# Kernel tuning notes

Hardware: AMD Instinct MI355X
Metric: run time of the kernel (lower is better)

## Reference

```python
import jax, jax.numpy as jnp
import numpy as np

B, D, K = 256, 1024, 128  # batch, num variables (leaves), units per node


def setup_inputs() -> dict:
    key = jax.random.key(0)
    k1, k2, k3, k4 = jax.random.split(key, 4)
    x = jax.random.normal(k1, (B, D), dtype=jnp.float32)
    mu = jax.random.normal(k2, (D, K), dtype=jnp.float32)
    log_sigma = 0.1 * jax.random.normal(k3, (D, K), dtype=jnp.float32)
    # log-weight logits for all 512+256+...+1 = 1023 inner sum nodes, concatenated
    weights = jax.random.normal(k4, (D - 1, K, K), dtype=jnp.float32)
    return {"x": x, "mu": mu, "log_sigma": log_sigma, "weights": weights}


def _log_matmul(y, logw):
    # y: [B, d, K] log-values; logw: [d, K, K] normalized log-weights (<= 0)
    # out[b,d,i] = logsumexp_j( logw[d,i,j] + y[b,d,j] ), computed without
    # materializing a [B,d,K,K] tensor: shift-by-max + linear-space matmul.
    m = jnp.max(y, axis=-1, keepdims=True)                  # [B, d, 1]
    e = jnp.exp(y - m)                                      # [B, d, K]
    s = jnp.einsum("bdj,dij->bdi", e, jnp.exp(logw))        # [B, d, K]
    return m + jnp.log(s)


def reference(x, mu, log_sigma, weights):
    # --- input (leaf) layer: per-variable Gaussian log-densities, [B, D, K] ---
    half_log_2pi = 0.5 * jnp.log(jnp.asarray(2.0 * np.pi, dtype=x.dtype))
    z = (x[:, :, None] - mu) * jnp.exp(-log_sigma)
    y = -0.5 * z * z - log_sigma - half_log_2pi             # [B, D, K]

    # --- topological sweep over the binary-tree DAG: product then sum layers ---
    off = 0
    d = y.shape[1]
    while d > 1:
        d //= 2
        # product nodes: sum log-probs of adjacent children -> [B, d, K]
        y = y[:, 0::2, :] + y[:, 1::2, :]
        # sum nodes: normalized log-space mixture over K child units
        logw = jax.nn.log_softmax(weights[off:off + d], axis=-1)  # [d, K, K]
        y = _log_matmul(y, logw)
        off += d
    return y[:, 0, :]  # root outputs, [B, K]
```

## Files before the change

kernel.cpp:

```cpp
#include <hip/hip_runtime.h>
#include <math.h>


#define DD 1024
#define KK 128
#define NT 256
#define HALF_LOG_2PI 0.9189385332046727f

typedef __attribute__((ext_vector_type(8))) short bf16x8;
typedef __attribute__((ext_vector_type(4))) float f32x4;

__device__ __forceinline__ unsigned short bf16_rn(float f) {
    unsigned u = __builtin_bit_cast(unsigned, f);
    u += 0x7fffu + ((u >> 16) & 1u);
    return (unsigned short)(u >> 16);
}
__device__ __forceinline__ float bf16f(unsigned short h) {
    unsigned u = ((unsigned)h) << 16;
    return __builtin_bit_cast(float, u);
}

template <int BT, bool LEAF>
__global__ __launch_bounds__(NT, 1) void spn_level(
    const float* __restrict__ x, const float* __restrict__ mu,
    const float* __restrict__ ls, const float* __restrict__ yprev,
    const float* __restrict__ weights, float* __restrict__ yout,
    int d, int woff)
{
    constexpr int JPT = NT / BT;
    constexpr int JW  = KK / JPT;

    extern __shared__ char smem[];
    unsigned short* Whi = (unsigned short*)smem;
    unsigned short* Wlo = Whi + 128 * 128;
    unsigned short* Ehi = Wlo + 128 * 128;
    unsigned short* Elo = Ehi + BT * 128;
    float* logrs = (float*)(Elo + BT * 128);
    float* mrow  = logrs + 128;
    float* redW  = mrow + BT;
    float* redE  = redW + NT;
    float* musig = redE + NT;

    const int n     = blockIdx.x;
    const int btile = blockIdx.y;
    const int t     = threadIdx.x;

    if (LEAF) {
        const int c = t >> 7, j = t & 127;
        const float lsv = ls[(size_t)(2 * n + c) * KK + j];
        musig[c * 128 + j]       = __expf(-lsv);
        musig[256 + c * 128 + j] = -lsv - HALF_LOG_2PI;
        musig[512 + c * 128 + j] = mu[(size_t)(2 * n + c) * KK + j];
    }
    {
        const int i = t >> 1;
        const int h = t & 1;
        const float* wg = weights + (((size_t)(woff + n)) << 14) + (i << 7) + (h << 6);
        const int sw = (i & 7) << 3;
        unsigned short* wh = Whi + i * 128;
        unsigned short* wl = Wlo + i * 128;
        float ps = 0.f;
        #pragma unroll
        for (int c = 0; c < 8; ++c) {
            float4 v0 = *(const float4*)(wg + 8 * c);
            float4 v1 = *(const float4*)(wg + 8 * c + 4);
            float e[8] = {__expf(v0.x), __expf(v0.y), __expf(v0.z), __expf(v0.w),
                          __expf(v1.x), __expf(v1.y), __expf(v1.z), __expf(v1.w)};
            bf16x8 hv, lv;
            #pragma unroll
            for (int q = 0; q < 8; ++q) {
                ps += e[q];
                const unsigned short hb = bf16_rn(e[q]);
                hv[q] = (short)hb;
                lv[q] = (short)bf16_rn(e[q] - bf16f(hb));
            }
            const int j0 = (h << 6) + 8 * c;
            *(bf16x8*)&wh[j0 ^ sw] = hv;
            *(bf16x8*)&wl[j0 ^ sw] = lv;
        }
        redW[t] = ps;
    }
    __syncthreads();

    if (t < 128) logrs[t] = __logf(redW[2 * t] + redW[2 * t + 1]);

    const int bl = t & (BT - 1);
    const int jh = t / BT;
    const int b  = btile * BT + bl;
    float p[JW];
    float lmax = -3.0e38f;
    if (LEAF) {
        const float xa = x[(size_t)b * DD + 2 * n];
        const float xb = x[(size_t)b * DD + 2 * n + 1];
        const float* isga = musig;        const float* isgb = musig + 128;
        const float* cta  = musig + 256;  const float* ctb  = musig + 384;
        const float* mva  = musig + 512;  const float* mvb  = musig + 640;
        #pragma unroll
        for (int c = 0; c < JW / 4; ++c) {
            const int j = jh * JW + 4 * c;
            const float4 ia = *(const float4*)(isga + j);
            const float4 ib = *(const float4*)(isgb + j);
            const float4 ca = *(const float4*)(cta + j);
            const float4 cb = *(const float4*)(ctb + j);
            const float4 ma = *(const float4*)(mva + j);
            const float4 mb = *(const float4*)(mvb + j);
            float za, zb, v;
            za = (xa - ma.x) * ia.x; zb = (xb - mb.x) * ib.x;
            v = fmaf(-0.5f * za, za, ca.x) + fmaf(-0.5f * zb, zb, cb.x);
            p[4 * c + 0] = v; lmax = fmaxf(lmax, v);
            za = (xa - ma.y) * ia.y; zb = (xb - mb.y) * ib.y;
            v = fmaf(-0.5f * za, za, ca.y) + fmaf(-0.5f * zb, zb, cb.y);
            p[4 * c + 1] = v; lmax = fmaxf(lmax, v);
            za = (xa - ma.z) * ia.z; zb = (xb - mb.z) * ib.z;
            v = fmaf(-0.5f * za, za, ca.z) + fmaf(-0.5f * zb, zb, cb.z);
            p[4 * c + 2] = v; lmax = fmaxf(lmax, v);
            za = (xa - ma.w) * ia.w; zb = (xb - mb.w) * ib.w;
            v = fmaf(-0.5f * za, za, ca.w) + fmaf(-0.5f * zb, zb, cb.w);
            p[4 * c + 3] = v; lmax = fmaxf(lmax, v);
        }
    } else {
        const float* ra = yprev + ((size_t)b * (2 * d) + 2 * n) * KK + jh * JW;
        const float* rb = ra + KK;
        #pragma unroll
        for (int c = 0; c < JW / 4; ++c) {
            const float4 a4 = *(const float4*)(ra + 4 * c);
            const float4 b4 = *(const float4*)(rb + 4 * c);
            const float p0 = a4.x + b4.x, p1 = a4.y + b4.y;
            const float p2 = a4.z + b4.z, p3 = a4.w + b4.w;
            p[4 * c + 0] = p0; p[4 * c + 1] = p1;
            p[4 * c + 2] = p2; p[4 * c + 3] = p3;
            lmax = fmaxf(lmax, fmaxf(fmaxf(p0, p1), fmaxf(p2, p3)));
        }
    }
    redE[t] = lmax;
    __syncthreads();

    if (t < BT) {
        float m = redE[t];
        #pragma unroll
        for (int q = 1; q < JPT; ++q) m = fmaxf(m, redE[t + BT * q]);
        mrow[t] = m;
    }
    float mx = redE[bl];
    #pragma unroll
    for (int q = 1; q < JPT; ++q) mx = fmaxf(mx, redE[bl + BT * q]);
    {
        const int sw = (bl & 7) << 3;
        unsigned short* eh = Ehi + bl * 128;
        unsigned short* el = Elo + bl * 128;
        #pragma unroll
        for (int c = 0; c < JW / 8; ++c) {
            bf16x8 hv, lv;
            #pragma unroll
            for (int q = 0; q < 8; ++q) {
                const float ev = __expf(p[8 * c + q] - mx);
                const unsigned short hb = bf16_rn(ev);
                hv[q] = (short)hb;
                lv[q] = (short)bf16_rn(ev - bf16f(hb));
            }
            const int j0 = jh * JW + 8 * c;
            *(bf16x8*)&eh[j0 ^ sw] = hv;
            *(bf16x8*)&el[j0 ^ sw] = lv;
        }
    }
    __syncthreads();

    const int w  = t >> 6;
    const int ln = t & 63;
    const int lr = ln & 15;
    const int lk = ln >> 4;
    constexpr int NWB = (BT == 128) ? 4 : 1;
    const int bt0 = (BT == 128) ? ((w >> 1) * 4) : (w & 1);
    const int it0 = (BT == 128) ? ((w & 1) * 4) : ((w >> 1) * 4);

    f32x4 acc[NWB][4];
    #pragma unroll
    for (int bi = 0; bi < NWB; ++bi)
        #pragma unroll
        for (int ci = 0; ci < 4; ++ci) acc[bi][ci] = (f32x4){0.f, 0.f, 0.f, 0.f};

    const int kb = lk * 8;
    #pragma unroll
    for (int ks = 0; ks < 4; ++ks) {
        const int jo = ks * 32 + kb;
        bf16x8 ah[NWB], al[NWB];
        #pragma unroll
        for (int bi = 0; bi < NWB; ++bi) {
            const int r = (bt0 + bi) * 16 + lr;
            const int idx = r * 128 + (jo ^ ((r & 7) << 3));
            ah[bi] = *(bf16x8*)&Ehi[idx];
            al[bi] = *(bf16x8*)&Elo[idx];
        }
        #pragma unroll
        for (int ci = 0; ci < 4; ++ci) {
            const int r = (it0 + ci) * 16 + lr;
            const int idx = r * 128 + (jo ^ ((r & 7) << 3));
            const bf16x8 bh = *(bf16x8*)&Whi[idx];
            const bf16x8 blo = *(bf16x8*)&Wlo[idx];
            #pragma unroll
            for (int bi = 0; bi < NWB; ++bi) {
                acc[bi][ci] = __builtin_amdgcn_mfma_f32_16x16x32_bf16(ah[bi], bh,  acc[bi][ci], 0, 0, 0);
                acc[bi][ci] = __builtin_amdgcn_mfma_f32_16x16x32_bf16(ah[bi], blo, acc[bi][ci], 0, 0, 0);
                acc[bi][ci] = __builtin_amdgcn_mfma_f32_16x16x32_bf16(al[bi], bh,  acc[bi][ci], 0, 0, 0);
            }
        }
    }

    #pragma unroll
    for (int bi = 0; bi < NWB; ++bi) {
        const int brl = (bt0 + bi) * 16 + lk * 4;
        #pragma unroll
        for (int ci = 0; ci < 4; ++ci) {
            const int ic = (it0 + ci) * 16 + lr;
            const float lrs = logrs[ic];
            const f32x4 a = acc[bi][ci];
            #pragma unroll
            for (int r = 0; r < 4; ++r) {
                const float m = mrow[brl + r];
                const size_t off = ((size_t)(btile * BT + brl + r) * d + n) * KK + ic;
                yout[off] = m + __logf(a[r]) - lrs;
            }
        }
    }
}

extern "C" void kernel_launch(void* const* d_in, const int* in_sizes, int n_in,
                              void* d_out, int out_size, void* d_ws, size_t ws_size,
                              hipStream_t stream) {
    const float* x  = (const float*)d_in[0];
    const float* mu = (const float*)d_in[1];
    const float* ls = (const float*)d_in[2];
    const float* w  = (const float*)d_in[3];
    float* out  = (float*)d_out;
    float* buf0 = (float*)d_ws;
    float* buf1 = buf0 + (size_t)256 * 512 * KK;

    const int sh128 = 65536 + 128 * 512 + 512 + 512 + 1024 + 1024 + 3072;
    const int sh32  = 65536 +  32 * 512 + 512 + 128 + 1024 + 1024 + 3072;

    (void)hipFuncSetAttribute((const void*)spn_level<128, true>,
                              hipFuncAttributeMaxDynamicSharedMemorySize, sh128);
    (void)hipFuncSetAttribute((const void*)spn_level<128, false>,
                              hipFuncAttributeMaxDynamicSharedMemorySize, sh128);
    (void)hipFuncSetAttribute((const void*)spn_level<32, false>,
                              hipFuncAttributeMaxDynamicSharedMemorySize, sh32);

    spn_level<128, true><<<dim3(512, 2), dim3(NT), sh128, stream>>>(
        x, mu, ls, nullptr, w, buf0, 512, 0);

    const float* src = buf0;
    float* other = buf1;
    int woff = 512;
    for (int d = 256; d >= 1; d >>= 1) {
        float* o = (d == 1) ? out : other;
        if (d >= 64) {
            spn_level<128, false><<<dim3(d, 2), dim3(NT), sh128, stream>>>(
                nullptr, nullptr, nullptr, src, w, o, d, woff);
        } else {
            spn_level<32, false><<<dim3(d, 8), dim3(NT), sh32, stream>>>(
                nullptr, nullptr, nullptr, src, w, o, d, woff);
        }
        woff += d;
        other = (float*)src;
        src = o;
    }
}
```

Measured before the change: 268.4 us.

## Precompute split-bf16 weights in a pre-pass and double threads per block

Adds a w_pre kernel that exponentiates all sum-node weights once, splits them into hi/lo bf16 planes in the swizzled layout, and stores per-row log-sums to workspace. The level kernels then copy these planes straight into LDS with global_load_lds instead of doing exp and conversion per block, which removes repeated transcendental work when several batch tiles share a node. Block size goes from 256 to 512 threads with launch bounds allowing 2 blocks per CU, and the MFMA work per wave is cut to match. The cost is an extra kernel launch and extra workspace traffic for the bf16 planes; the fused path remains as a fallback when the workspace is too small.

```diff
diff --git a/kernel.cpp b/kernel.cpp
--- a/kernel.cpp
+++ b/kernel.cpp
@@ -4,7 +4,7 @@
 
 #define DD 1024
 #define KK 128
-#define NT 256
+#define NT 512
 #define HALF_LOG_2PI 0.9189385332046727f
 
 typedef __attribute__((ext_vector_type(8))) short bf16x8;
@@ -19,12 +19,54 @@
     unsigned u = ((unsigned)h) << 16;
     return __builtin_bit_cast(float, u);
 }
-
-template <int BT, bool LEAF>
-__global__ __launch_bounds__(NT, 1) void spn_level(
+__device__ __forceinline__ void gload_lds16(const void* g, void* l) {
+    __builtin_amdgcn_global_load_lds(
+        (const __attribute__((address_space(1))) unsigned int*)g,
+        (__attribute__((address_space(3))) unsigned int*)l, 16, 0, 0);
+}
+
+__global__ __launch_bounds__(256, 4) void w_pre(
+    const float* __restrict__ weights, unsigned short* __restrict__ wpl,
+    float* __restrict__ lrs)
+{
+    __shared__ float red[256];
+    const int node = blockIdx.x;
+    const int t = threadIdx.x;
+    const int i = t >> 1, h = t & 1;
+    const float* wg = weights + ((size_t)node << 14) + (i << 7) + (h << 6);
+    unsigned short* wh = wpl + ((size_t)node << 15) + i * 128;
+    unsigned short* wl = wh + 16384;
+    const int sw = (i & 7) << 3;
+    float ps = 0.f;
+    #pragma unroll
+    for (int c = 0; c < 8; ++c) {
+        float4 v0 = *(const float4*)(wg + 8 * c);
+        float4 v1 = *(const float4*)(wg + 8 * c + 4);
+        float e[8] = {__expf(v0.x), __expf(v0.y), __expf(v0.z), __expf(v0.w),
+                      __expf(v1.x), __expf(v1.y), __expf(v1.z), __expf(v1.w)};
+        bf16x8 hv, lv;
+        #pragma unroll
+        for (int q = 0; q < 8; ++q) {
+            ps += e[q];
+            const unsigned short hb = bf16_rn(e[q]);
+            hv[q] = (short)hb;
+            lv[q] = (short)bf16_rn(e[q] - bf16f(hb));
+        }
+        const int j0 = (h << 6) + 8 * c;
+        *(bf16x8*)&wh[j0 ^ sw] = hv;
+        *(bf16x8*)&wl[j0 ^ sw] = lv;
+    }
+    red[t] = ps;
+    __syncthreads();
+    if (t < 128) lrs[(size_t)node * 128 + t] = __logf(red[2 * t] + red[2 * t + 1]);
+}
+
+template <int BT, bool LEAF, bool PRE>
+__global__ __launch_bounds__(NT, 2) void spn_level(
     const float* __restrict__ x, const float* __restrict__ mu,
     const float* __restrict__ ls, const float* __restrict__ yprev,
-    const float* __restrict__ weights, float* __restrict__ yout,
+    const float* __restrict__ weights, const unsigned short* __restrict__ wpl,
+    const float* __restrict__ lrsg, float* __restrict__ yout,
     int d, int woff)
 {
     constexpr int JPT = NT / BT;
@@ -32,36 +74,37 @@
 
     extern __shared__ char smem[];
     unsigned short* Whi = (unsigned short*)smem;
-    unsigned short* Wlo = Whi + 128 * 128;
-    unsigned short* Ehi = Wlo + 128 * 128;
+    unsigned short* Wlo = Whi + 16384;
+    unsigned short* Ehi = Wlo + 16384;
     unsigned short* Elo = Ehi + BT * 128;
     float* logrs = (float*)(Elo + BT * 128);
     float* mrow  = logrs + 128;
-    float* redW  = mrow + BT;
-    float* redE  = redW + NT;
-    float* musig = redE + NT;
+    float* redE  = mrow + BT;
+    float* redW  = redE + NT;
+    float* musig = redW + NT;
 
     const int n     = blockIdx.x;
     const int btile = blockIdx.y;
     const int t     = threadIdx.x;
-
-    if (LEAF) {
-        const int c = t >> 7, j = t & 127;
-        const float lsv = ls[(size_t)(2 * n + c) * KK + j];
-        musig[c * 128 + j]       = __expf(-lsv);
-        musig[256 + c * 128 + j] = -lsv - HALF_LOG_2PI;
-        musig[512 + c * 128 + j] = mu[(size_t)(2 * n + c) * KK + j];
-    }
-    {
-        const int i = t >> 1;
-        const int h = t & 1;
-        const float* wg = weights + (((size_t)(woff + n)) << 14) + (i << 7) + (h << 6);
-        const int sw = (i & 7) << 3;
+    const int node  = woff + n;
+
+    if (PRE) {
+        const int wv = t >> 6, ln = t & 63;
+        const char* gsrc = (const char*)(wpl + ((size_t)node << 15)) + wv * 8192 + (size_t)ln * 16;
+        char* ldst = (char*)Whi + wv * 8192;
+        #pragma unroll
+        for (int q = 0; q < 8; ++q)
+            gload_lds16(gsrc + q * 1024, ldst + q * 1024);
+        if (t < 128) logrs[t] = lrsg[(size_t)node * 128 + t];
+    } else {
+        const int i = t >> 2, h = t & 3;
+        const float* wg = weights + ((size_t)node << 14) + (i << 7) + (h << 5);
         unsigned short* wh = Whi + i * 128;
         unsigned short* wl = Wlo + i * 128;
+        const int sw = (i & 7) << 3;
         float ps = 0.f;
         #pragma unroll
-        for (int c = 0; c < 8; ++c) {
+        for (int c = 0; c < 4; ++c) {
             float4 v0 = *(const float4*)(wg + 8 * c);
             float4 v1 = *(const float4*)(wg + 8 * c + 4);
             float e[8] = {__expf(v0.x), __expf(v0.y), __expf(v0.z), __expf(v0.w),
@@ -74,15 +117,23 @@
                 hv[q] = (short)hb;
                 lv[q] = (short)bf16_rn(e[q] - bf16f(hb));
             }
-            const int j0 = (h << 6) + 8 * c;
+            const int j0 = (h << 5) + 8 * c;
             *(bf16x8*)&wh[j0 ^ sw] = hv;
             *(bf16x8*)&wl[j0 ^ sw] = lv;
         }
         redW[t] = ps;
     }
+    if (LEAF && t < 256) {
+        const int c = t >> 7, j = t & 127;
+        const float lsv = ls[(size_t)(2 * n + c) * KK + j];
+        musig[c * 128 + j]       = __expf(-lsv);
+        musig[256 + c * 128 + j] = -lsv - HALF_LOG_2PI;
+        musig[512 + c * 128 + j] = mu[(size_t)(2 * n + c) * KK + j];
+    }
     __syncthreads();
 
-    if (t < 128) logrs[t] = __logf(redW[2 * t] + redW[2 * t + 1]);
+    if (!PRE && t < 128)
+        logrs[t] = __logf(redW[4 * t] + redW[4 * t + 1] + redW[4 * t + 2] + redW[4 * t + 3]);
 
     const int bl = t & (BT - 1);
     const int jh = t / BT;
@@ -165,19 +216,22 @@
     }
     __syncthreads();
 
-    const int w  = t >> 6;
+    const int wv = t >> 6;
     const int ln = t & 63;
     const int lr = ln & 15;
     const int lk = ln >> 4;
-    constexpr int NWB = (BT == 128) ? 4 : 1;
-    const int bt0 = (BT == 128) ? ((w >> 1) * 4) : (w & 1);
-    const int it0 = (BT == 128) ? ((w & 1) * 4) : ((w >> 1) * 4);
-
-    f32x4 acc[NWB][4];
+    constexpr int NWB = (BT == 128) ? 2 : 1;
+    constexpr int NCI = (BT == 128) ? 4 : 2;
+    const int wr = (BT == 128) ? (wv >> 1) : (wv & 1);
+    const int wc = (BT == 128) ? (wv & 1) : (wv >> 1);
+    const int bt0 = wr * NWB;
+    const int it0 = wc * NCI;
+
+    f32x4 acc[NWB][NCI];
     #pragma unroll
     for (int bi = 0; bi < NWB; ++bi)
         #pragma unroll
-        for (int ci = 0; ci < 4; ++ci) acc[bi][ci] = (f32x4){0.f, 0.f, 0.f, 0.f};
+        for (int ci = 0; ci < NCI; ++ci) acc[bi][ci] = (f32x4){0.f, 0.f, 0.f, 0.f};
 
     const int kb = lk * 8;
     #pragma unroll
@@ -192,10 +246,10 @@
             al[bi] = *(bf16x8*)&Elo[idx];
         }
         #pragma unroll
-        for (int ci = 0; ci < 4; ++ci) {
+        for (int ci = 0; ci < NCI; ++ci) {
             const int r = (it0 + ci) * 16 + lr;
             const int idx = r * 128 + (jo ^ ((r & 7) << 3));
-            const bf16x8 bh = *(bf16x8*)&Whi[idx];
+            const bf16x8 bh  = *(bf16x8*)&Whi[idx];
             const bf16x8 blo = *(bf16x8*)&Wlo[idx];
             #pragma unroll
             for (int bi = 0; bi < NWB; ++bi) {
@@ -210,15 +264,15 @@
     for (int bi = 0; bi < NWB; ++bi) {
         const int brl = (bt0 + bi) * 16 + lk * 4;
         #pragma unroll
-        for (int ci = 0; ci < 4; ++ci) {
+        for (int ci = 0; ci < NCI; ++ci) {
             const int ic = (it0 + ci) * 16 + lr;
-            const float lrs = logrs[ic];
+            const float lrsv = logrs[ic];
             const f32x4 a = acc[bi][ci];
             #pragma unroll
             for (int r = 0; r < 4; ++r) {
                 const float m = mrow[brl + r];
                 const size_t off = ((size_t)(btile * BT + brl + r) * d + n) * KK + ic;
-                yout[off] = m + __logf(a[r]) - lrs;
+                yout[off] = m + __logf(a[r]) - lrsv;
             }
         }
     }
@@ -234,19 +288,31 @@
     float* out  = (float*)d_out;
     float* buf0 = (float*)d_ws;
     float* buf1 = buf0 + (size_t)256 * 512 * KK;
-
-    const int sh128 = 65536 + 128 * 512 + 512 + 512 + 1024 + 1024 + 3072;
-    const int sh32  = 65536 +  32 * 512 + 512 + 128 + 1024 + 1024 + 3072;
-
-    (void)hipFuncSetAttribute((const void*)spn_level<128, true>,
-                              hipFuncAttributeMaxDynamicSharedMemorySize, sh128);
-    (void)hipFuncSetAttribute((const void*)spn_level<128, false>,
-                              hipFuncAttributeMaxDynamicSharedMemorySize, sh128);
-    (void)hipFuncSetAttribute((const void*)spn_level<32, false>,
-                              hipFuncAttributeMaxDynamicSharedMemorySize, sh32);
-
-    spn_level<128, true><<<dim3(512, 2), dim3(NT), sh128, stream>>>(
-        x, mu, ls, nullptr, w, buf0, 512, 0);
+    unsigned short* wpl = (unsigned short*)(buf1 + (size_t)256 * 256 * KK);
+    float* lrs = (float*)(wpl + (size_t)1023 * 32768);
+
+    const size_t NEED = ((size_t)(256 * 512 * 128) + (size_t)(256 * 256 * 128)) * 4
+                      + (size_t)1023 * 32768 * 2 + (size_t)1023 * 128 * 4;
+    const bool pre = ws_size >= NEED;
+
+    const int shA = 65536 + 65536 + 512 + 512 + NT * 4 + NT * 4 + 3072;
+    const int shB = 65536 + 16384 + 512 + 128 + NT * 4 + NT * 4;
+
+    (void)hipFuncSetAttribute((const void*)spn_level<128, true,  true >, hipFuncAttributeMaxDynamicSharedMemorySize, shA);
+    (void)hipFuncSetAttribute((const void*)spn_level<128, true,  false>, hipFuncAttributeMaxDynamicSharedMemorySize, shA);
+    (void)hipFuncSetAttribute((const void*)spn_level<128, false, true >, hipFuncAttributeMaxDynamicSharedMemorySize, shA);
+    (void)hipFuncSetAttribute((const void*)spn_level<128, false, false>, hipFuncAttributeMaxDynamicSharedMemorySize, shA);
+    (void)hipFuncSetAttribute((const void*)spn_level<32,  false, true >, hipFuncAttributeMaxDynamicSharedMemorySize, shB);
+    (void)hipFuncSetAttribute((const void*)spn_level<32,  false, false>, hipFuncAttributeMaxDynamicSharedMemorySize, shB);
+
+    if (pre) w_pre<<<dim3(1023), dim3(256), 0, stream>>>(w, wpl, lrs);
+
+    if (pre)
+        spn_level<128, true, true><<<dim3(512, 2), dim3(NT), shA, stream>>>(
+            x, mu, ls, nullptr, w, wpl, lrs, buf0, 512, 0);
+    else
+        spn_level<128, true, false><<<dim3(512, 2), dim3(NT), shA, stream>>>(
+            x, mu, ls, nullptr, w, wpl, lrs, buf0, 512, 0);
 
     const float* src = buf0;
     float* other = buf1;
@@ -254,11 +320,19 @@
     for (int d = 256; d >= 1; d >>= 1) {
         float* o = (d == 1) ? out : other;
         if (d >= 64) {
-            spn_level<128, false><<<dim3(d, 2), dim3(NT), sh128, stream>>>(
-                nullptr, nullptr, nullptr, src, w, o, d, woff);
+            if (pre)
+                spn_level<128, false, true><<<dim3(d, 2), dim3(NT), shA, stream>>>(
+                    nullptr, nullptr, nullptr, src, w, wpl, lrs, o, d, woff);
+            else
+                spn_level<128, false, false><<<dim3(d, 2), dim3(NT), shA, stream>>>(
+                    nullptr, nullptr, nullptr, src, w, wpl, lrs, o, d, woff);
         } else {
-            spn_level<32, false><<<dim3(d, 8), dim3(NT), sh32, stream>>>(
-                nullptr, nullptr, nullptr, src, w, o, d, woff);
+            if (pre)
+                spn_level<32, false, true><<<dim3(d, 8), dim3(NT), shB, stream>>>(
+                    nullptr, nullptr, nullptr, src, w, wpl, lrs, o, d, woff);
+            else
+                spn_level<32, false, false><<<dim3(d, 8), dim3(NT), shB, stream>>>(
+                    nullptr, nullptr, nullptr, src, w, wpl, lrs, o, d, woff);
         }
         woff += d;
         other = (float*)src;
```

After: 299.7 us. 1.12x slower.

## Build MFMA A-fragments in registers and drop the E shared tile

Applied to the files above, without the earlier changes.

Each wave now computes the product/leaf log-values directly in the MFMA A-operand lane layout, takes the row max with register reductions and cross-lane shuffles, and converts to split bf16 fragments in registers. This removes the E hi/lo shared-memory tiles, two block barriers and the shared-memory max reduction. Blocks grow to 512 threads for the 128-row case, the weight row-sum reduction uses shuffles, and launch bounds request 4 blocks per CU. Shared memory per block shrinks, which may allow higher occupancy. In exchange, each wave register-holds 32 values plus fragments, and the waves that share a row tile each recompute that tile's exps.

```diff
diff --git a/kernel.cpp b/kernel.cpp
--- a/kernel.cpp
+++ b/kernel.cpp
@@ -4,7 +4,6 @@
 
 #define DD 1024
 #define KK 128
-#define NT 256
 #define HALF_LOG_2PI 0.9189385332046727f
 
 typedef __attribute__((ext_vector_type(8))) short bf16x8;
@@ -20,50 +19,42 @@
     return __builtin_bit_cast(float, u);
 }
 
-template <int BT, bool LEAF>
-__global__ __launch_bounds__(NT, 1) void spn_level(
+template <int BT, int NTH, bool LEAF>
+__global__ __launch_bounds__(NTH, 4) void spn_level(
     const float* __restrict__ x, const float* __restrict__ mu,
     const float* __restrict__ ls, const float* __restrict__ yprev,
     const float* __restrict__ weights, float* __restrict__ yout,
     int d, int woff)
 {
-    constexpr int JPT = NT / BT;
-    constexpr int JW  = KK / JPT;
+    constexpr int NW  = NTH / 64;
+    constexpr int NRT = BT / 16;
+    constexpr int WPR = NW / NRT;
+    constexpr int NCI = 8 / WPR;
 
     extern __shared__ char smem[];
     unsigned short* Whi = (unsigned short*)smem;
-    unsigned short* Wlo = Whi + 128 * 128;
-    unsigned short* Ehi = Wlo + 128 * 128;
-    unsigned short* Elo = Ehi + BT * 128;
-    float* logrs = (float*)(Elo + BT * 128);
-    float* mrow  = logrs + 128;
-    float* redW  = mrow + BT;
-    float* redE  = redW + NT;
-    float* musig = redE + NT;
+    unsigned short* Wlo = Whi + 16384;
+    float* logrs = (float*)(Wlo + 16384);
+    float* musig = logrs + 128;
 
     const int n     = blockIdx.x;
     const int btile = blockIdx.y;
     const int t     = threadIdx.x;
-
-    if (LEAF) {
-        const int c = t >> 7, j = t & 127;
-        const float lsv = ls[(size_t)(2 * n + c) * KK + j];
-        musig[c * 128 + j]       = __expf(-lsv);
-        musig[256 + c * 128 + j] = -lsv - HALF_LOG_2PI;
-        musig[512 + c * 128 + j] = mu[(size_t)(2 * n + c) * KK + j];
-    }
+    const int node  = woff + n;
+
     {
-        const int i = t >> 1;
-        const int h = t & 1;
-        const float* wg = weights + (((size_t)(woff + n)) << 14) + (i << 7) + (h << 6);
-        const int sw = (i & 7) << 3;
+        constexpr int TPR = NTH / 128;
+        constexpr int EPT = 128 / TPR;
+        const int i = t / TPR, h = t % TPR;
+        const float* wr = weights + ((size_t)node << 14) + i * 128 + h * EPT;
         unsigned short* wh = Whi + i * 128;
         unsigned short* wl = Wlo + i * 128;
+        const int sw = (i & 7) << 3;
         float ps = 0.f;
         #pragma unroll
-        for (int c = 0; c < 8; ++c) {
-            float4 v0 = *(const float4*)(wg + 8 * c);
-            float4 v1 = *(const float4*)(wg + 8 * c + 4);
+        for (int c = 0; c < EPT / 8; ++c) {
+            float4 v0 = *(const float4*)(wr + 8 * c);
+            float4 v1 = *(const float4*)(wr + 8 * c + 4);
             float e[8] = {__expf(v0.x), __expf(v0.y), __expf(v0.z), __expf(v0.w),
                           __expf(v1.x), __expf(v1.y), __expf(v1.z), __expf(v1.w)};
             bf16x8 hv, lv;
@@ -74,94 +65,20 @@
                 hv[q] = (short)hb;
                 lv[q] = (short)bf16_rn(e[q] - bf16f(hb));
             }
-            const int j0 = (h << 6) + 8 * c;
+            const int j0 = h * EPT + 8 * c;
             *(bf16x8*)&wh[j0 ^ sw] = hv;
             *(bf16x8*)&wl[j0 ^ sw] = lv;
         }
-        redW[t] = ps;
-    }
-    __syncthreads();
-
-    if (t < 128) logrs[t] = __logf(redW[2 * t] + redW[2 * t + 1]);
-
-    const int bl = t & (BT - 1);
-    const int jh = t / BT;
-    const int b  = btile * BT + bl;
-    float p[JW];
-    float lmax = -3.0e38f;
-    if (LEAF) {
-        const float xa = x[(size_t)b * DD + 2 * n];
-        const float xb = x[(size_t)b * DD + 2 * n + 1];
-        const float* isga = musig;        const float* isgb = musig + 128;
-        const float* cta  = musig + 256;  const float* ctb  = musig + 384;
-        const float* mva  = musig + 512;  const float* mvb  = musig + 640;
-        #pragma unroll
-        for (int c = 0; c < JW / 4; ++c) {
-            const int j = jh * JW + 4 * c;
-            const float4 ia = *(const float4*)(isga + j);
-            const float4 ib = *(const float4*)(isgb + j);
-            const float4 ca = *(const float4*)(cta + j);
-            const float4 cb = *(const float4*)(ctb + j);
-            const float4 ma = *(const float4*)(mva + j);
-            const float4 mb = *(const float4*)(mvb + j);
-            float za, zb, v;
-            za = (xa - ma.x) * ia.x; zb = (xb - mb.x) * ib.x;
-            v = fmaf(-0.5f * za, za, ca.x) + fmaf(-0.5f * zb, zb, cb.x);
-            p[4 * c + 0] = v; lmax = fmaxf(lmax, v);
-            za = (xa - ma.y) * ia.y; zb = (xb - mb.y) * ib.y;
-            v = fmaf(-0.5f * za, za, ca.y) + fmaf(-0.5f * zb, zb, cb.y);
-            p[4 * c + 1] = v; lmax = fmaxf(lmax, v);
-            za = (xa - ma.z) * ia.z; zb = (xb - mb.z) * ib.z;
-            v = fmaf(-0.5f * za, za, ca.z) + fmaf(-0.5f * zb, zb, cb.z);
-            p[4 * c + 2] = v; lmax = fmaxf(lmax, v);
-            za = (xa - ma.w) * ia.w; zb = (xb - mb.w) * ib.w;
-            v = fmaf(-0.5f * za, za, ca.w) + fmaf(-0.5f * zb, zb, cb.w);
-            p[4 * c + 3] = v; lmax = fmaxf(lmax, v);
-        }
-    } else {
-        const float* ra = yprev + ((size_t)b * (2 * d) + 2 * n) * KK + jh * JW;
-        const float* rb = ra + KK;
-        #pragma unroll
-        for (int c = 0; c < JW / 4; ++c) {
-            const float4 a4 = *(const float4*)(ra + 4 * c);
-            const float4 b4 = *(const float4*)(rb + 4 * c);
-            const float p0 = a4.x + b4.x, p1 = a4.y + b4.y;
-            const float p2 = a4.z + b4.z, p3 = a4.w + b4.w;
-            p[4 * c + 0] = p0; p[4 * c + 1] = p1;
-            p[4 * c + 2] = p2; p[4 * c + 3] = p3;
-            lmax = fmaxf(lmax, fmaxf(fmaxf(p0, p1), fmaxf(p2, p3)));
-        }
-    }
-    redE[t] = lmax;
-    __syncthreads();
-
-    if (t < BT) {
-        float m = redE[t];
-        #pragma unroll
-        for (int q = 1; q < JPT; ++q) m = fmaxf(m, redE[t + BT * q]);
-        mrow[t] = m;
-    }
-    float mx = redE[bl];
-    #pragma unroll
-    for (int q = 1; q < JPT; ++q) mx = fmaxf(mx, redE[bl + BT * q]);
-    {
-        const int sw = (bl & 7) << 3;
-        unsigned short* eh = Ehi + bl * 128;
-        unsigned short* el = Elo + bl * 128;
-        #pragma unroll
-        for (int c = 0; c < JW / 8; ++c) {
-            bf16x8 hv, lv;
-            #pragma unroll
-            for (int q = 0; q < 8; ++q) {
-                const float ev = __expf(p[8 * c + q] - mx);
-                const unsigned short hb = bf16_rn(ev);
-                hv[q] = (short)hb;
-                lv[q] = (short)bf16_rn(ev - bf16f(hb));
-            }
-            const int j0 = jh * JW + 8 * c;
-            *(bf16x8*)&eh[j0 ^ sw] = hv;
-            *(bf16x8*)&el[j0 ^ sw] = lv;
-        }
+        #pragma unroll
+        for (int s2 = 1; s2 < TPR; s2 <<= 1) ps += __shfl_xor(ps, s2);
+        if (h == 0) logrs[i] = __logf(ps);
+    }
+    if (LEAF && t < 256) {
+        const int c = t >> 7, j = t & 127;
+        const float lsv = ls[(size_t)(2 * n + c) * KK + j];
+        musig[c * 128 + j]       = __expf(-lsv);
+        musig[256 + c * 128 + j] = -lsv - HALF_LOG_2PI;
+        musig[512 + c * 128 + j] = mu[(size_t)(2 * n + c) * KK + j];
     }
     __syncthreads();
 
@@ -169,57 +86,107 @@
     const int ln = t & 63;
     const int lr = ln & 15;
     const int lk = ln >> 4;
-    constexpr int NWB = (BT == 128) ? 4 : 1;
-    const int bt0 = (BT == 128) ? ((w >> 1) * 4) : (w & 1);
-    const int it0 = (BT == 128) ? ((w & 1) * 4) : ((w >> 1) * 4);
-
-    f32x4 acc[NWB][4];
-    #pragma unroll
-    for (int bi = 0; bi < NWB; ++bi)
-        #pragma unroll
-        for (int ci = 0; ci < 4; ++ci) acc[bi][ci] = (f32x4){0.f, 0.f, 0.f, 0.f};
-
-    const int kb = lk * 8;
+    const int rt  = w / WPR;
+    const int ci0 = (w % WPR) * NCI;
+    const int brow = btile * BT + rt * 16 + lr;
+
+    float p[32];
+    if (LEAF) {
+        const float xa = x[(size_t)brow * DD + 2 * n];
+        const float xb = x[(size_t)brow * DD + 2 * n + 1];
+        #pragma unroll
+        for (int ks = 0; ks < 4; ++ks) {
+            #pragma unroll
+            for (int g = 0; g < 2; ++g) {
+                const int j = ks * 32 + lk * 8 + 4 * g;
+                const float4 ia = *(const float4*)&musig[j];
+                const float4 ib = *(const float4*)&musig[128 + j];
+                const float4 ca = *(const float4*)&musig[256 + j];
+                const float4 cb = *(const float4*)&musig[384 + j];
+                const float4 ma = *(const float4*)&musig[512 + j];
+                const float4 mb = *(const float4*)&musig[640 + j];
+                float za, zb;
+                za = (xa - ma.x) * ia.x; zb = (xb - mb.x) * ib.x;
+                p[ks * 8 + 4 * g + 0] = fmaf(-0.5f * za, za, ca.x) + fmaf(-0.5f * zb, zb, cb.x);
+                za = (xa - ma.y) * ia.y; zb = (xb - mb.y) * ib.y;
+                p[ks * 8 + 4 * g + 1] = fmaf(-0.5f * za, za, ca.y) + fmaf(-0.5f * zb, zb, cb.y);
+                za = (xa - ma.z) * ia.z; zb = (xb - mb.z) * ib.z;
+                p[ks * 8 + 4 * g + 2] = fmaf(-0.5f * za, za, ca.z) + fmaf(-0.5f * zb, zb, cb.z);
+                za = (xa - ma.w) * ia.w; zb = (xb - mb.w) * ib.w;
+                p[ks * 8 + 4 * g + 3] = fmaf(-0.5f * za, za, ca.w) + fmaf(-0.5f * zb, zb, cb.w);
+            }
+        }
+    } else {
+        const float* ra = yprev + ((size_t)brow * (2 * d) + 2 * n) * KK;
+        #pragma unroll
+        for (int ks = 0; ks < 4; ++ks) {
+            const int j0 = ks * 32 + lk * 8;
+            const float4 a0 = *(const float4*)(ra + j0);
+            const float4 a1 = *(const float4*)(ra + j0 + 4);
+            const float4 b0 = *(const float4*)(ra + KK + j0);
+            const float4 b1 = *(const float4*)(ra + KK + j0 + 4);
+            p[ks * 8 + 0] = a0.x + b0.x; p[ks * 8 + 1] = a0.y + b0.y;
+            p[ks * 8 + 2] = a0.z + b0.z; p[ks * 8 + 3] = a0.w + b0.w;
+            p[ks * 8 + 4] = a1.x + b1.x; p[ks * 8 + 5] = a1.y + b1.y;
+            p[ks * 8 + 6] = a1.z + b1.z; p[ks * 8 + 7] = a1.w + b1.w;
+        }
+    }
+
+    float m16[16];
+    #pragma unroll
+    for (int q = 0; q < 16; ++q) m16[q] = fmaxf(p[q], p[q + 16]);
+    float m8[8];
+    #pragma unroll
+    for (int q = 0; q < 8; ++q) m8[q] = fmaxf(m16[q], m16[q + 8]);
+    float m4a[4];
+    #pragma unroll
+    for (int q = 0; q < 4; ++q) m4a[q] = fmaxf(m8[q], m8[q + 4]);
+    float mx = fmaxf(fmaxf(m4a[0], m4a[1]), fmaxf(m4a[2], m4a[3]));
+    mx = fmaxf(mx, __shfl_xor(mx, 16));
+    mx = fmaxf(mx, __shfl_xor(mx, 32));
+
+    bf16x8 ah[4], al[4];
     #pragma unroll
     for (int ks = 0; ks < 4; ++ks) {
-        const int jo = ks * 32 + kb;
-        bf16x8 ah[NWB], al[NWB];
-        #pragma unroll
-        for (int bi = 0; bi < NWB; ++bi) {
-            const int r = (bt0 + bi) * 16 + lr;
-            const int idx = r * 128 + (jo ^ ((r & 7) << 3));
-            ah[bi] = *(bf16x8*)&Ehi[idx];
-            al[bi] = *(bf16x8*)&Elo[idx];
-        }
-        #pragma unroll
-        for (int ci = 0; ci < 4; ++ci) {
-            const int r = (it0 + ci) * 16 + lr;
-            const int idx = r * 128 + (jo ^ ((r & 7) << 3));
+        #pragma unroll
+        for (int q = 0; q < 8; ++q) {
+            const float ev = __expf(p[ks * 8 + q] - mx);
+            const unsigned short hb = bf16_rn(ev);
+            ah[ks][q] = (short)hb;
+            al[ks][q] = (short)bf16_rn(ev - bf16f(hb));
+        }
+    }
+
+    f32x4 acc[NCI];
+    #pragma unroll
+    for (int ci = 0; ci < NCI; ++ci) acc[ci] = (f32x4){0.f, 0.f, 0.f, 0.f};
+    #pragma unroll
+    for (int ci = 0; ci < NCI; ++ci) {
+        const int i = (ci0 + ci) * 16 + lr;
+        const int base = i * 128;
+        const int sw = (i & 7) << 3;
+        #pragma unroll
+        for (int ks = 0; ks < 4; ++ks) {
+            const int idx = base + ((ks * 32 + lk * 8) ^ sw);
             const bf16x8 bh = *(bf16x8*)&Whi[idx];
-            const bf16x8 blo = *(bf16x8*)&Wlo[idx];
-            #pragma unroll
-            for (int bi = 0; bi < NWB; ++bi) {
-                acc[bi][ci] = __builtin_amdgcn_mfma_f32_16x16x32_bf16(ah[bi], bh,  acc[bi][ci], 0, 0, 0);
-                acc[bi][ci] = __builtin_amdgcn_mfma_f32_16x16x32_bf16(ah[bi], blo, acc[bi][ci], 0, 0, 0);
-                acc[bi][ci] = __builtin_amdgcn_mfma_f32_16x16x32_bf16(al[bi], bh,  acc[bi][ci], 0, 0, 0);
-            }
-        }
-    }
-
-    #pragma unroll
-    for (int bi = 0; bi < NWB; ++bi) {
-        const int brl = (bt0 + bi) * 16 + lk * 4;
-        #pragma unroll
-        for (int ci = 0; ci < 4; ++ci) {
-            const int ic = (it0 + ci) * 16 + lr;
-            const float lrs = logrs[ic];
-            const f32x4 a = acc[bi][ci];
-            #pragma unroll
-            for (int r = 0; r < 4; ++r) {
-                const float m = mrow[brl + r];
-                const size_t off = ((size_t)(btile * BT + brl + r) * d + n) * KK + ic;
-                yout[off] = m + __logf(a[r]) - lrs;
-            }
+            const bf16x8 bl = *(bf16x8*)&Wlo[idx];
+            acc[ci] = __builtin_amdgcn_mfma_f32_16x16x32_bf16(ah[ks], bh, acc[ci], 0, 0, 0);
+            acc[ci] = __builtin_amdgcn_mfma_f32_16x16x32_bf16(ah[ks], bl, acc[ci], 0, 0, 0);
+            acc[ci] = __builtin_amdgcn_mfma_f32_16x16x32_bf16(al[ks], bh, acc[ci], 0, 0, 0);
+        }
+    }
+
+    float mv4[4];
+    #pragma unroll
+    for (int r = 0; r < 4; ++r) mv4[r] = __shfl(mx, lk * 4 + r);
+    #pragma unroll
+    for (int ci = 0; ci < NCI; ++ci) {
+        const int icol = (ci0 + ci) * 16 + lr;
+        const float lrsv = logrs[icol];
+        #pragma unroll
+        for (int r = 0; r < 4; ++r) {
+            const int b = btile * BT + rt * 16 + lk * 4 + r;
+            yout[((size_t)b * d + n) * KK + icol] = mv4[r] + __logf(acc[ci][r]) - lrsv;
         }
     }
 }
@@ -235,17 +202,17 @@
     float* buf0 = (float*)d_ws;
     float* buf1 = buf0 + (size_t)256 * 512 * KK;
 
-    const int sh128 = 65536 + 128 * 512 + 512 + 512 + 1024 + 1024 + 3072;
-    const int sh32  = 65536 +  32 * 512 + 512 + 128 + 1024 + 1024 + 3072;
-
-    (void)hipFuncSetAttribute((const void*)spn_level<128, true>,
-                              hipFuncAttributeMaxDynamicSharedMemorySize, sh128);
-    (void)hipFuncSetAttribute((const void*)spn_level<128, false>,
-                              hipFuncAttributeMaxDynamicSharedMemorySize, sh128);
-    (void)hipFuncSetAttribute((const void*)spn_level<32, false>,
-                              hipFuncAttributeMaxDynamicSharedMemorySize, sh32);
-
-    spn_level<128, true><<<dim3(512, 2), dim3(NT), sh128, stream>>>(
+    const int shBig   = 65536 + 512 + 3072;
+    const int shSmall = 65536 + 512;
+
+    (void)hipFuncSetAttribute((const void*)spn_level<128, 512, true>,
+                              hipFuncAttributeMaxDynamicSharedMemorySize, shBig);
+    (void)hipFuncSetAttribute((const void*)spn_level<128, 512, false>,
+                              hipFuncAttributeMaxDynamicSharedMemorySize, shBig);
+    (void)hipFuncSetAttribute((const void*)spn_level<32, 256, false>,
+                              hipFuncAttributeMaxDynamicSharedMemorySize, shSmall);
+
+    spn_level<128, 512, true><<<dim3(512, 2), dim3(512), shBig, stream>>>(
         x, mu, ls, nullptr, w, buf0, 512, 0);
 
     const float* src = buf0;
@@ -254,10 +221,10 @@
     for (int d = 256; d >= 1; d >>= 1) {
         float* o = (d == 1) ? out : other;
         if (d >= 64) {
-            spn_level<128, false><<<dim3(d, 2), dim3(NT), sh128, stream>>>(
+            spn_level<128, 512, false><<<dim3(d, 2), dim3(512), shBig, stream>>>(
                 nullptr, nullptr, nullptr, src, w, o, d, woff);
         } else {
-            spn_level<32, false><<<dim3(d, 8), dim3(NT), sh32, stream>>>(
+            spn_level<32, 256, false><<<dim3(d, 8), dim3(256), shSmall, stream>>>(
                 nullptr, nullptr, nullptr, src, w, o, d, woff);
         }
         woff += d;
```

Result: faster. 245.3 us (-8.6%).
